# Kernel optimization log

Measured on AMD Instinct MI355X. Metric: run time of the kernel, lower is better.

The kernel has to match this reference:

```python
import jax, jax.numpy as jnp
import numpy as np

FACTOR = 5  # init arg 'factor'


def setup_inputs() -> dict:
    key = jax.random.key(0)
    ks = jax.random.split(key, 9)
    B, L, H, D = 32, 4096, 8, 64
    sh = (B, L, H, D)
    scale = 0.125  # 1/sqrt(D)
    return {
        "queries": jax.random.normal(ks[0], sh, jnp.float32),
        "keys": jax.random.normal(ks[1], sh, jnp.float32),
        "values": jax.random.normal(ks[2], sh, jnp.float32),
        "Wq": jax.random.normal(ks[3], (1, D), jnp.float32) * scale,
        "bq": jax.random.normal(ks[4], (1,), jnp.float32) * scale,
        "Wk": jax.random.normal(ks[5], (1, D), jnp.float32) * scale,
        "bk": jax.random.normal(ks[6], (1,), jnp.float32) * scale,
        "Wv": jax.random.normal(ks[7], (1, D), jnp.float32) * scale,
        "bv": jax.random.normal(ks[8], (1,), jnp.float32) * scale,
    }


def reference(queries, keys, values, Wq, bq, Wk, bk, Wv, bv):
    B, L_Q, H, D = queries.shape
    # transpose(2,1) + LazyLinear(1) + squeeze  ->  scalar series per (b, h, t)
    q = jnp.einsum('blhd,d->bhl', queries, Wq[0]) + bq[0]  # [B,H,L_Q]
    k = jnp.einsum('blhd,d->bhl', keys, Wk[0]) + bk[0]
    v = jnp.einsum('blhd,d->bhl', values, Wv[0]) + bv[0]
    # L_K == L_Q here: torch takes the last L_Q steps (identity in this config)
    k = k[:, :, -L_Q:]
    v = v[:, :, -L_Q:]
    # FFT cross-correlation scores (rfft with n=2L-1 -> L bins; irfft default -> 2L-2)
    n_fft = 2 * L_Q - 1
    Qf = jnp.fft.rfft(q, n_fft)
    Kf = jnp.conj(jnp.fft.rfft(k, n_fft))
    score = jnp.fft.irfft(Qf * Kf)[:, :, :L_Q] / L_Q  # [B,H,L_Q]
    kk = FACTOR * int(np.ceil(np.log(L_Q)))  # 45 for L_Q=4096
    weight, top_idx = jax.lax.top_k(score, kk)  # [B,H,kk]
    weight = jax.nn.softmax(weight, axis=-1)
    # torch: indices = L_Q - top_idx - 1; rolled-V row j is roll(v, j+1),
    # i.e. shift = L_Q - top_idx, so V_sel[b,h,d,t] = v[b,h,(t + top_idx[b,h,d]) % L_Q].
    t = jnp.arange(L_Q)
    gidx = (top_idx[..., None] + t[None, None, None, :]) % L_Q  # [B,H,kk,L_Q]
    V_sel = jnp.take_along_axis(v[:, :, None, :], gidx, axis=-1)  # [B,H,kk,L_Q]
    out = jnp.einsum('bhd,bhdl->bhl', weight, V_sel)  # [B,H,L_Q]
    return out[..., None]  # [B,H,L_Q,1]
```

## Files before the change

### kernel.cpp

```cpp
#include <hip/hip_runtime.h>
#include <math.h>
#include <float.h>

#define L_   4096
#define M_   8192
#define H_   8
#define D_   64
#define KK   45

#define WS_C   0
#define WS_D   4096
#define WS_TW  8192
#define WS_H1  16384
#define WS_H2  24576
#define WS_QKV 32768

__device__ __forceinline__ float2 cadd(float2 a, float2 b) { return make_float2(a.x + b.x, a.y + b.y); }
__device__ __forceinline__ float2 csub(float2 a, float2 b) { return make_float2(a.x - b.x, a.y - b.y); }
__device__ __forceinline__ float2 cmulf(float2 a, float2 b) {
  return make_float2(a.x * b.x - a.y * b.y, a.x * b.y + a.y * b.x);
}
__device__ __forceinline__ float2 cmulcf(float2 a, float2 b) {
  return make_float2(a.x * b.x + a.y * b.y, a.y * b.x - a.x * b.y);
}

__device__ __forceinline__ float2 twf(int e) {
  float s, c;
  __sincosf((float)e * -7.66990394e-4f, &s, &c);
  return make_float2(c, s);
}

#define R4DIF(BUF) { \
  const float2 a = BUF[i0], b = BUF[i0 + q], c = BUF[i0 + 2 * q], d = BUF[i0 + 3 * q]; \
  const float2 t0 = cadd(a, c), t1 = csub(a, c), t2 = cadd(b, d), t3 = csub(b, d); \
  BUF[i0]         = cadd(t0, t2); \
  BUF[i0 + q]     = cmulf(make_float2(t1.x + t3.y, t1.y - t3.x), w1); \
  BUF[i0 + 2 * q] = cmulf(csub(t0, t2), w2); \
  BUF[i0 + 3 * q] = cmulf(make_float2(t1.x - t3.y, t1.y + t3.x), w3); }

#define R4DIT(BUF) { \
  const float2 z0 = BUF[i0]; \
  const float2 z1 = cmulcf(BUF[i0 + q],     w1); \
  const float2 z2 = cmulcf(BUF[i0 + 2 * q], w2); \
  const float2 z3 = cmulcf(BUF[i0 + 3 * q], w3); \
  const float2 t0 = cadd(z0, z2), t1 = csub(z0, z2), t2 = cadd(z1, z3), u = csub(z1, z3); \
  BUF[i0]         = cadd(t0, t2); \
  BUF[i0 + q]     = make_float2(t1.x - u.y, t1.y + u.x); \
  BUF[i0 + 2 * q] = csub(t0, t2); \
  BUF[i0 + 3 * q] = make_float2(t1.x + u.y, t1.y - u.x); }

__device__ __forceinline__ float4 midpair(float4 a, float4 h) {
  float2 u = make_float2(a.x + a.z, a.y + a.w);
  float2 v = make_float2(a.x - a.z, a.y - a.w);
  u = cmulf(u, make_float2(h.x, h.y));
  v = cmulf(v, make_float2(h.z, h.w));
  return make_float4(u.x + v.x, u.y + v.y, u.x - v.x, u.y - v.y);
}

static __device__ void conv2(float2* A, float2* B, const float2* __restrict__ Hf) {
  const int tid = threadIdx.x;
  #pragma unroll
  for (int s = 0; s < 6; ++s) {
    const int q = 2048 >> (2 * s);
    __syncthreads();
    #pragma unroll
    for (int r = 0; r < 2; ++r) {
      const int bid = tid + (r << 10);
      const int j   = bid & (q - 1);
      const int i0  = ((bid >> (11 - 2 * s)) << (13 - 2 * s)) + j;
      const float2 w1 = twf(j << (2 * s));
      const float2 w2 = cmulf(w1, w1);
      const float2 w3 = cmulf(w2, w1);
      R4DIF(A) R4DIF(B)
    }
  }
  __syncthreads();
  #pragma unroll
  for (int r = 0; r < 4; ++r) {
    const int p = tid + (r << 10);
    const float4 h = reinterpret_cast<const float4*>(Hf)[p];
    reinterpret_cast<float4*>(A)[p] = midpair(reinterpret_cast<float4*>(A)[p], h);
    reinterpret_cast<float4*>(B)[p] = midpair(reinterpret_cast<float4*>(B)[p], h);
  }
  #pragma unroll
  for (int s = 5; s >= 0; --s) {
    const int q = 2048 >> (2 * s);
    __syncthreads();
    #pragma unroll
    for (int r = 0; r < 2; ++r) {
      const int bid = tid + (r << 10);
      const int j   = bid & (q - 1);
      const int i0  = ((bid >> (11 - 2 * s)) << (13 - 2 * s)) + j;
      const float2 w1 = twf(j << (2 * s));
      const float2 w2 = cmulf(w1, w1);
      const float2 w3 = cmulf(w2, w1);
      R4DIT(A) R4DIT(B)
    }
  }
  __syncthreads();
}

static __device__ void conv1(float2* A, const float2* __restrict__ Hf) {
  const int tid = threadIdx.x;
  #pragma unroll
  for (int s = 0; s < 6; ++s) {
    const int q = 2048 >> (2 * s);
    __syncthreads();
    #pragma unroll
    for (int r = 0; r < 2; ++r) {
      const int bid = tid + (r << 10);
      const int j   = bid & (q - 1);
      const int i0  = ((bid >> (11 - 2 * s)) << (13 - 2 * s)) + j;
      const float2 w1 = twf(j << (2 * s));
      const float2 w2 = cmulf(w1, w1);
      const float2 w3 = cmulf(w2, w1);
      R4DIF(A)
    }
  }
  __syncthreads();
  #pragma unroll
  for (int r = 0; r < 4; ++r) {
    const int p = tid + (r << 10);
    const float4 h = reinterpret_cast<const float4*>(Hf)[p];
    reinterpret_cast<float4*>(A)[p] = midpair(reinterpret_cast<float4*>(A)[p], h);
  }
  #pragma unroll
  for (int s = 5; s >= 0; --s) {
    const int q = 2048 >> (2 * s);
    __syncthreads();
    #pragma unroll
    for (int r = 0; r < 2; ++r) {
      const int bid = tid + (r << 10);
      const int j   = bid & (q - 1);
      const int i0  = ((bid >> (11 - 2 * s)) << (13 - 2 * s)) + j;
      const float2 w1 = twf(j << (2 * s));
      const float2 w2 = cmulf(w1, w1);
      const float2 w3 = cmulf(w2, w1);
      R4DIT(A)
    }
  }
  __syncthreads();
}

template <int NT>
static __device__ void fft_dif_tab(float2* buf, const float2* __restrict__ tw) {
  const int tid = threadIdx.x;
  for (int s = 0; s < 6; ++s) {
    const int q = 2048 >> (2 * s);
    __syncthreads();
    for (int r = 0; r < 2048 / NT; ++r) {
      const int bid = tid + r * NT;
      const int j   = bid & (q - 1);
      const int i0  = ((bid >> (11 - 2 * s)) << (13 - 2 * s)) + j;
      const int e   = j << (2 * s);
      const float2 w1 = tw[e], w2 = tw[2 * e], w3 = tw[3 * e];
      R4DIF(buf)
    }
  }
  __syncthreads();
  for (int r = 0; r < 4096 / NT; ++r) {
    const int i0 = (tid + r * NT) << 1;
    const float2 a = buf[i0], b = buf[i0 + 1];
    buf[i0] = cadd(a, b); buf[i0 + 1] = csub(a, b);
  }
  __syncthreads();
}

extern "C" __global__ void setup_tables(float2* ws) {
  const int idx = blockIdx.x * 512 + threadIdx.x;
  if (idx < 4096) {
    const long p = ((long)idx * idx) % 16382;
    const double th = -M_PI * (double)p / 8191.0;
    double s, c; sincos(th, &s, &c);
    ws[WS_C + idx] = make_float2((float)c, (float)s);
  } else if (idx < 8192) {
    const int j = idx - 4096;
    const long p = ((long)j * j) % 16380;
    const double th = M_PI * (double)p / 8190.0;
    double s, c; sincos(th, &s, &c);
    ws[WS_D + j] = make_float2((float)c, (float)s);
  } else if (idx < 16384) {
    const int j = idx - 8192;
    const double th = -M_PI * (double)j / 4096.0;
    double s, c; sincos(th, &s, &c);
    ws[WS_TW + j] = make_float2((float)c, (float)s);
  }
}

extern "C" __global__ __launch_bounds__(512, 1) void setup_filters(float2* ws) {
  __shared__ __align__(16) float2 buf[M_];
  const float2* src = ws + (blockIdx.x == 0 ? WS_C : WS_D);
  float2*       dst = ws + (blockIdx.x == 0 ? WS_H1 : WS_H2);
  const float2* tw  = ws + WS_TW;
  for (int i = threadIdx.x; i < M_; i += 512) {
    float2 val = make_float2(0.f, 0.f);
    if (i != 4096) {
      const int jj = (i <= 4095) ? i : (M_ - i);
      const float2 e = src[jj];
      val = make_float2(e.x, -e.y);
    }
    buf[i] = val;
  }
  fft_dif_tab<512>(buf, tw);
  const float sc = 1.0f / 8192.0f;
  for (int i = threadIdx.x; i < M_; i += 512)
    dst[i] = make_float2(buf[i].x * sc, buf[i].y * sc);
}

extern "C" __global__ __launch_bounds__(256)
void proj_kernel(const float* __restrict__ queries, const float* __restrict__ keys,
                 const float* __restrict__ values,
                 const float* __restrict__ Wq, const float* __restrict__ bq,
                 const float* __restrict__ Wk, const float* __restrict__ bk,
                 const float* __restrict__ Wv, const float* __restrict__ bv,
                 float* __restrict__ q_ws, float* __restrict__ k_ws,
                 float* __restrict__ v_ws)
{
  const int tid  = threadIdx.x;
  const int wave = tid >> 6;
  const int lane = tid & 63;
  const int qt   = lane & 3;
  const int rr   = lane >> 2;
  const int hh   = rr & 7;
  const int dl   = rr >> 3;
  const int blk  = blockIdx.x;
  const int b    = blk >> 6;
  const int lbase = (blk & 63) << 6;

  const float* srcs[3] = {queries, keys, values};
  const float* Wsx[3]  = {Wq, Wk, Wv};
  const float* Bsx[3]  = {bq, bk, bv};
  float* dsts[3] = {q_ws, k_ws, v_ws};

  #pragma unroll
  for (int s = 0; s < 3; ++s) {
    const float4* src4 = reinterpret_cast<const float4*>(srcs[s]) + (size_t)b * 524288;
    const float4* W4   = reinterpret_cast<const float4*>(Wsx[s]);
    float4 w[4];
    #pragma unroll
    for (int j = 0; j < 4; ++j) w[j] = W4[qt * 4 + j];
    const float bias = Bsx[s][0];
    float* dst = dsts[s] + ((size_t)(b * 8 + hh) << 12);

    #pragma unroll
    for (int st = 0; st < 4; ++st) {
      const int l0a = lbase + st * 16 + wave * 2;
      const int l0b = l0a + 8;
      const float4* pa = src4 + (size_t)l0a * 128 + lane * 4;
      const float4* pb = src4 + (size_t)l0b * 128 + lane * 4;
      float4 xa[4], xb[4];
      #pragma unroll
      for (int j = 0; j < 4; ++j) xa[j] = pa[j];
      #pragma unroll
      for (int j = 0; j < 4; ++j) xb[j] = pb[j];
      float fa = 0.f, fb = 0.f;
      #pragma unroll
      for (int j = 0; j < 4; ++j) {
        fa += xa[j].x * w[j].x + xa[j].y * w[j].y + xa[j].z * w[j].z + xa[j].w * w[j].w;
        fb += xb[j].x * w[j].x + xb[j].y * w[j].y + xb[j].z * w[j].z + xb[j].w * w[j].w;
      }
      fa += __shfl_xor(fa, 1); fb += __shfl_xor(fb, 1);
      fa += __shfl_xor(fa, 2); fb += __shfl_xor(fb, 2);
      if (qt == 0) {
        dst[l0a + dl] = fa + bias;
        dst[l0b + dl] = fb + bias;
      }
    }
  }
}

extern "C" __global__ __launch_bounds__(1024, 1)
void autocorr_main(const float2* __restrict__ ws,
                   const float* __restrict__ q_ws, const float* __restrict__ k_ws,
                   const float* __restrict__ v_ws, float* __restrict__ outp)
{
  __shared__ __align__(16) float2 bufA[M_];
  __shared__ __align__(16) float2 bufB[M_];
  __shared__ float  v_lds[L_];
  __shared__ float  cand_v[16 * KK];
  __shared__ int    cand_i[16 * KK];
  __shared__ float  w_sh[KK];
  __shared__ int    i_sh[KK];

  const int tid = threadIdx.x;
  const int bh  = blockIdx.x;

  const float2* c_t = ws + WS_C;
  const float2* d_t = ws + WS_D;
  const float2* H1  = ws + WS_H1;
  const float2* H2  = ws + WS_H2;
  const float* qrow = q_ws + ((size_t)bh << 12);
  const float* krow = k_ws + ((size_t)bh << 12);
  const float* vrow = v_ws + ((size_t)bh << 12);

  {
    const float4 v4 = reinterpret_cast<const float4*>(vrow)[tid];
    reinterpret_cast<float4*>(v_lds)[tid] = v4;
    const float4 k4 = reinterpret_cast<const float4*>(krow)[tid];
    const float4 q4 = reinterpret_cast<const float4*>(qrow)[tid];
    const float4 c01 = reinterpret_cast<const float4*>(c_t)[2 * tid];
    const float4 c23 = reinterpret_cast<const float4*>(c_t)[2 * tid + 1];
    float4* A4 = reinterpret_cast<float4*>(bufA);
    float4* B4 = reinterpret_cast<float4*>(bufB);
    A4[2 * tid]     = make_float4(k4.x * c01.x, k4.x * c01.y, k4.y * c01.z, k4.y * c01.w);
    A4[2 * tid + 1] = make_float4(k4.z * c23.x, k4.z * c23.y, k4.w * c23.z, k4.w * c23.w);
    B4[2 * tid]     = make_float4(q4.x * c01.x, q4.x * c01.y, q4.y * c01.z, q4.y * c01.w);
    B4[2 * tid + 1] = make_float4(q4.z * c23.x, q4.z * c23.y, q4.w * c23.z, q4.w * c23.w);
    const float4 z = make_float4(0.f, 0.f, 0.f, 0.f);
    A4[2048 + tid] = z; A4[3072 + tid] = z;
    B4[2048 + tid] = z; B4[3072 + tid] = z;
  }

  conv2(bufA, bufB, H1);

  #pragma unroll
  for (int r = 0; r < 4; ++r) {
    const int m = tid + (r << 10);
    const float2 cc = c_t[m];
    const float2 K = cmulf(cc, bufA[m]);
    const float2 Q = cmulf(cc, bufB[m]);
    const float2 F = cmulcf(Q, K);
    float2 g;
    if (m == 0 || m == 4095) g = make_float2(F.x, 0.f);
    else                     g = make_float2(2.f * F.x, 2.f * F.y);
    bufA[m] = cmulf(g, d_t[m]);
  }
  #pragma unroll
  for (int r = 4; r < 8; ++r) bufA[tid + (r << 10)] = make_float2(0.f, 0.f);

  conv1(bufA, H2);

  const float SCALE = (float)(1.0 / (8190.0 * 4096.0));
  float svv[4]; int sii[4];
  #pragma unroll
  for (int r = 0; r < 4; ++r) {
    const int t = tid + (r << 10);
    const float2 Z = cmulf(d_t[t], bufA[t]);
    svv[r] = Z.x * SCALE;
    sii[r] = t;
  }
  const int lane = tid & 63, wv = tid >> 6;
  for (int it = 0; it < KK; ++it) {
    float bvv = -FLT_MAX; int bii = 0x7fffffff;
    #pragma unroll
    for (int c = 0; c < 4; ++c)
      if (svv[c] > bvv || (svv[c] == bvv && sii[c] < bii)) { bvv = svv[c]; bii = sii[c]; }
    #pragma unroll
    for (int off = 1; off < 64; off <<= 1) {
      const float ov = __shfl_xor(bvv, off);
      const int   oi = __shfl_xor(bii, off);
      if (ov > bvv || (ov == bvv && oi < bii)) { bvv = ov; bii = oi; }
    }
    #pragma unroll
    for (int c = 0; c < 4; ++c) if (sii[c] == bii) svv[c] = -FLT_MAX;
    if (lane == 0) { cand_v[wv * KK + it] = bvv; cand_i[wv * KK + it] = bii; }
  }
  __syncthreads();

  if (tid < 64) {
    float mv[12]; int mi[12];
    #pragma unroll
    for (int c = 0; c < 12; ++c) {
      const int id = tid + 64 * c;
      if (id < 16 * KK) { mv[c] = cand_v[id]; mi[c] = cand_i[id]; }
      else              { mv[c] = -FLT_MAX;   mi[c] = 0x7fffffff; }
    }
    float m0 = 0.f, sum = 0.f, myv = -FLT_MAX; int myi = 0;
    for (int it = 0; it < KK; ++it) {
      float bvv = -FLT_MAX; int bii = 0x7fffffff;
      #pragma unroll
      for (int c = 0; c < 12; ++c)
        if (mv[c] > bvv || (mv[c] == bvv && mi[c] < bii)) { bvv = mv[c]; bii = mi[c]; }
      #pragma unroll
      for (int off = 1; off < 64; off <<= 1) {
        const float ov = __shfl_xor(bvv, off);
        const int   oi = __shfl_xor(bii, off);
        if (ov > bvv || (ov == bvv && oi < bii)) { bvv = ov; bii = oi; }
      }
      if (it == 0) m0 = bvv;
      sum += expf(bvv - m0);
      if (tid == it) { myv = bvv; myi = bii; }
      #pragma unroll
      for (int c = 0; c < 12; ++c) if (mi[c] == bii) mv[c] = -FLT_MAX;
    }
    if (tid < KK) { w_sh[tid] = expf(myv - m0) / sum; i_sh[tid] = myi; }
  }
  __syncthreads();

  {
    float acc[4] = {0, 0, 0, 0};
    for (int j = 0; j < KK; ++j) {
      const float wj = w_sh[j];
      const int   bse = i_sh[j] + tid;
      #pragma unroll
      for (int r = 0; r < 4; ++r)
        acc[r] = fmaf(wj, v_lds[(bse + (r << 10)) & (L_ - 1)], acc[r]);
    }
    float* op = outp + ((size_t)bh << 12);
    #pragma unroll
    for (int r = 0; r < 4; ++r) op[tid + (r << 10)] = acc[r];
  }
}

extern "C" void kernel_launch(void* const* d_in, const int* in_sizes, int n_in,
                              void* d_out, int out_size, void* d_ws, size_t ws_size,
                              hipStream_t stream) {
  const float* queries = (const float*)d_in[0];
  const float* keys    = (const float*)d_in[1];
  const float* values  = (const float*)d_in[2];
  const float* Wq = (const float*)d_in[3];
  const float* bq = (const float*)d_in[4];
  const float* Wk = (const float*)d_in[5];
  const float* bk = (const float*)d_in[6];
  const float* Wv = (const float*)d_in[7];
  const float* bv = (const float*)d_in[8];
  float2* ws = (float2*)d_ws;
  float* q_ws = (float*)d_ws + 2 * WS_QKV;
  float* k_ws = q_ws + (1 << 20);
  float* v_ws = k_ws + (1 << 20);
  float* out = (float*)d_out;

  hipLaunchKernelGGL(setup_tables,  dim3(32), dim3(512), 0, stream, ws);
  hipLaunchKernelGGL(setup_filters, dim3(2),  dim3(512), 0, stream, ws);
  hipLaunchKernelGGL(proj_kernel,   dim3(2048), dim3(256), 0, stream,
                     queries, keys, values, Wq, bq, Wk, bk, Wv, bv, q_ws, k_ws, v_ws);
  hipLaunchKernelGGL(autocorr_main, dim3(256), dim3(1024), 0, stream,
                     ws, q_ws, k_ws, v_ws, out);
}
```

Baseline: 340.0 us.

## Swizzle LDS FFT buffers against bank conflicts and pipeline projection loads

The in-LDS radix-4 FFT buffers get an XOR-swizzled index mapping (PS/PS4), applied consistently to the butterfly stages, the pointwise multiply, the fill and the readout. The goal is to remove LDS bank conflicts on the strided butterfly accesses. The projection kernel is also rewritten as a triple-buffered software pipeline using nontemporal vector loads and a launch-bounds occupancy hint, so global loads overlap the dot-product reductions. The risks are extra index arithmetic, more register pressure, and subtle errors if any access to the buffers is missed by the swizzle.

New measurement: 396.9 us. +16.7%, slower.

```diff
diff --git a/kernel.cpp b/kernel.cpp
--- a/kernel.cpp
+++ b/kernel.cpp
@@ -15,6 +15,8 @@
 #define WS_H2  24576
 #define WS_QKV 32768
 
+typedef float vf4 __attribute__((ext_vector_type(4)));
+
 __device__ __forceinline__ float2 cadd(float2 a, float2 b) { return make_float2(a.x + b.x, a.y + b.y); }
 __device__ __forceinline__ float2 csub(float2 a, float2 b) { return make_float2(a.x - b.x, a.y - b.y); }
 __device__ __forceinline__ float2 cmulf(float2 a, float2 b) {
@@ -30,7 +32,10 @@
   return make_float2(c, s);
 }
 
-#define R4DIF(BUF) { \
+__device__ __forceinline__ int PS(int i)  { return i ^ ((i >> 3) & 0xE); }
+__device__ __forceinline__ int PS4(int t) { return t ^ ((t >> 3) & 7);  }
+
+#define R4DIF_L(BUF) { \
   const float2 a = BUF[i0], b = BUF[i0 + q], c = BUF[i0 + 2 * q], d = BUF[i0 + 3 * q]; \
   const float2 t0 = cadd(a, c), t1 = csub(a, c), t2 = cadd(b, d), t3 = csub(b, d); \
   BUF[i0]         = cadd(t0, t2); \
@@ -38,16 +43,24 @@
   BUF[i0 + 2 * q] = cmulf(csub(t0, t2), w2); \
   BUF[i0 + 3 * q] = cmulf(make_float2(t1.x - t3.y, t1.y + t3.x), w3); }
 
-#define R4DIT(BUF) { \
-  const float2 z0 = BUF[i0]; \
-  const float2 z1 = cmulcf(BUF[i0 + q],     w1); \
-  const float2 z2 = cmulcf(BUF[i0 + 2 * q], w2); \
-  const float2 z3 = cmulcf(BUF[i0 + 3 * q], w3); \
+#define R4DIFS(BUF) { \
+  const float2 a = BUF[a0], b = BUF[a1], c = BUF[a2], d = BUF[a3]; \
+  const float2 t0 = cadd(a, c), t1 = csub(a, c), t2 = cadd(b, d), t3 = csub(b, d); \
+  BUF[a0] = cadd(t0, t2); \
+  BUF[a1] = cmulf(make_float2(t1.x + t3.y, t1.y - t3.x), w1); \
+  BUF[a2] = cmulf(csub(t0, t2), w2); \
+  BUF[a3] = cmulf(make_float2(t1.x - t3.y, t1.y + t3.x), w3); }
+
+#define R4DITS(BUF) { \
+  const float2 z0 = BUF[a0]; \
+  const float2 z1 = cmulcf(BUF[a1], w1); \
+  const float2 z2 = cmulcf(BUF[a2], w2); \
+  const float2 z3 = cmulcf(BUF[a3], w3); \
   const float2 t0 = cadd(z0, z2), t1 = csub(z0, z2), t2 = cadd(z1, z3), u = csub(z1, z3); \
-  BUF[i0]         = cadd(t0, t2); \
-  BUF[i0 + q]     = make_float2(t1.x - u.y, t1.y + u.x); \
-  BUF[i0 + 2 * q] = csub(t0, t2); \
-  BUF[i0 + 3 * q] = make_float2(t1.x + u.y, t1.y - u.x); }
+  BUF[a0] = cadd(t0, t2); \
+  BUF[a1] = make_float2(t1.x - u.y, t1.y + u.x); \
+  BUF[a2] = csub(t0, t2); \
+  BUF[a3] = make_float2(t1.x + u.y, t1.y - u.x); }
 
 __device__ __forceinline__ float4 midpair(float4 a, float4 h) {
   float2 u = make_float2(a.x + a.z, a.y + a.w);
@@ -59,42 +72,50 @@
 
 static __device__ void conv2(float2* A, float2* B, const float2* __restrict__ Hf) {
   const int tid = threadIdx.x;
+  float4* A4f = reinterpret_cast<float4*>(A);
+  float4* B4f = reinterpret_cast<float4*>(B);
+  const float4* H4 = reinterpret_cast<const float4*>(Hf);
   #pragma unroll
   for (int s = 0; s < 6; ++s) {
     const int q = 2048 >> (2 * s);
+    const int pq1 = PS(q), pq2 = PS(2 * q), pq3 = PS(3 * q);
     __syncthreads();
     #pragma unroll
     for (int r = 0; r < 2; ++r) {
       const int bid = tid + (r << 10);
       const int j   = bid & (q - 1);
       const int i0  = ((bid >> (11 - 2 * s)) << (13 - 2 * s)) + j;
+      const int a0  = PS(i0), a1 = a0 ^ pq1, a2 = a0 ^ pq2, a3 = a0 ^ pq3;
       const float2 w1 = twf(j << (2 * s));
       const float2 w2 = cmulf(w1, w1);
       const float2 w3 = cmulf(w2, w1);
-      R4DIF(A) R4DIF(B)
+      R4DIFS(A) R4DIFS(B)
     }
   }
   __syncthreads();
   #pragma unroll
   for (int r = 0; r < 4; ++r) {
-    const int p = tid + (r << 10);
-    const float4 h = reinterpret_cast<const float4*>(Hf)[p];
-    reinterpret_cast<float4*>(A)[p] = midpair(reinterpret_cast<float4*>(A)[p], h);
-    reinterpret_cast<float4*>(B)[p] = midpair(reinterpret_cast<float4*>(B)[p], h);
+    const int p  = tid + (r << 10);
+    const int pp = PS4(p);
+    const float4 h = H4[p];
+    A4f[pp] = midpair(A4f[pp], h);
+    B4f[pp] = midpair(B4f[pp], h);
   }
   #pragma unroll
   for (int s = 5; s >= 0; --s) {
     const int q = 2048 >> (2 * s);
+    const int pq1 = PS(q), pq2 = PS(2 * q), pq3 = PS(3 * q);
     __syncthreads();
     #pragma unroll
     for (int r = 0; r < 2; ++r) {
       const int bid = tid + (r << 10);
       const int j   = bid & (q - 1);
       const int i0  = ((bid >> (11 - 2 * s)) << (13 - 2 * s)) + j;
+      const int a0  = PS(i0), a1 = a0 ^ pq1, a2 = a0 ^ pq2, a3 = a0 ^ pq3;
       const float2 w1 = twf(j << (2 * s));
       const float2 w2 = cmulf(w1, w1);
       const float2 w3 = cmulf(w2, w1);
-      R4DIT(A) R4DIT(B)
+      R4DITS(A) R4DITS(B)
     }
   }
   __syncthreads();
@@ -102,41 +123,48 @@
 
 static __device__ void conv1(float2* A, const float2* __restrict__ Hf) {
   const int tid = threadIdx.x;
+  float4* A4f = reinterpret_cast<float4*>(A);
+  const float4* H4 = reinterpret_cast<const float4*>(Hf);
   #pragma unroll
   for (int s = 0; s < 6; ++s) {
     const int q = 2048 >> (2 * s);
+    const int pq1 = PS(q), pq2 = PS(2 * q), pq3 = PS(3 * q);
     __syncthreads();
     #pragma unroll
     for (int r = 0; r < 2; ++r) {
       const int bid = tid + (r << 10);
       const int j   = bid & (q - 1);
       const int i0  = ((bid >> (11 - 2 * s)) << (13 - 2 * s)) + j;
+      const int a0  = PS(i0), a1 = a0 ^ pq1, a2 = a0 ^ pq2, a3 = a0 ^ pq3;
       const float2 w1 = twf(j << (2 * s));
       const float2 w2 = cmulf(w1, w1);
       const float2 w3 = cmulf(w2, w1);
-      R4DIF(A)
+      R4DIFS(A)
     }
   }
   __syncthreads();
   #pragma unroll
   for (int r = 0; r < 4; ++r) {
-    const int p = tid + (r << 10);
-    const float4 h = reinterpret_cast<const float4*>(Hf)[p];
-    reinterpret_cast<float4*>(A)[p] = midpair(reinterpret_cast<float4*>(A)[p], h);
+    const int p  = tid + (r << 10);
+    const int pp = PS4(p);
+    const float4 h = H4[p];
+    A4f[pp] = midpair(A4f[pp], h);
   }
   #pragma unroll
   for (int s = 5; s >= 0; --s) {
     const int q = 2048 >> (2 * s);
+    const int pq1 = PS(q), pq2 = PS(2 * q), pq3 = PS(3 * q);
     __syncthreads();
     #pragma unroll
     for (int r = 0; r < 2; ++r) {
       const int bid = tid + (r << 10);
       const int j   = bid & (q - 1);
       const int i0  = ((bid >> (11 - 2 * s)) << (13 - 2 * s)) + j;
+      const int a0  = PS(i0), a1 = a0 ^ pq1, a2 = a0 ^ pq2, a3 = a0 ^ pq3;
       const float2 w1 = twf(j << (2 * s));
       const float2 w2 = cmulf(w1, w1);
       const float2 w3 = cmulf(w2, w1);
-      R4DIT(A)
+      R4DITS(A)
     }
   }
   __syncthreads();
@@ -154,7 +182,7 @@
       const int i0  = ((bid >> (11 - 2 * s)) << (13 - 2 * s)) + j;
       const int e   = j << (2 * s);
       const float2 w1 = tw[e], w2 = tw[2 * e], w3 = tw[3 * e];
-      R4DIF(buf)
+      R4DIF_L(buf)
     }
   }
   __syncthreads();
@@ -207,7 +235,32 @@
     dst[i] = make_float2(buf[i].x * sc, buf[i].y * sc);
 }
 
-extern "C" __global__ __launch_bounds__(256)
+#define PROJ_ISSUE(BUF, IT) { \
+  const int s_ = (IT) >> 3, g_ = (IT) & 7; \
+  const int l0_ = lbase + (wave << 1) + (g_ << 3); \
+  const vf4* p_ = (s_ == 0 ? q4p : (s_ == 1 ? k4p : v4p)) + (((size_t)l0_) << 7) + (lane << 2); \
+  BUF[0] = __builtin_nontemporal_load(p_ + 0); \
+  BUF[1] = __builtin_nontemporal_load(p_ + 1); \
+  BUF[2] = __builtin_nontemporal_load(p_ + 2); \
+  BUF[3] = __builtin_nontemporal_load(p_ + 3); }
+
+#define PROJ_REDUCE(BUF, IT) { \
+  const int s_ = (IT) >> 3, g_ = (IT) & 7; \
+  const int l0_ = lbase + (wave << 1) + (g_ << 3); \
+  const float4 w0_ = (s_ == 0 ? wq0 : (s_ == 1 ? wk0 : wv0)); \
+  const float4 w1_ = (s_ == 0 ? wq1 : (s_ == 1 ? wk1 : wv1)); \
+  const float4 w2_ = (s_ == 0 ? wq2 : (s_ == 1 ? wk2 : wv2)); \
+  const float4 w3_ = (s_ == 0 ? wq3 : (s_ == 1 ? wk3 : wv3)); \
+  float f_ = BUF[0].x * w0_.x + BUF[0].y * w0_.y + BUF[0].z * w0_.z + BUF[0].w * w0_.w \
+           + BUF[1].x * w1_.x + BUF[1].y * w1_.y + BUF[1].z * w1_.z + BUF[1].w * w1_.w \
+           + BUF[2].x * w2_.x + BUF[2].y * w2_.y + BUF[2].z * w2_.z + BUF[2].w * w2_.w \
+           + BUF[3].x * w3_.x + BUF[3].y * w3_.y + BUF[3].z * w3_.z + BUF[3].w * w3_.w; \
+  f_ += __shfl_xor(f_, 1); f_ += __shfl_xor(f_, 2); \
+  if (qt == 0) { \
+    float* d_ = (s_ == 0 ? q_ws : (s_ == 1 ? k_ws : v_ws)) + (((size_t)(b8 + hh)) << 12) + l0_ + dl; \
+    *d_ = f_ + (s_ == 0 ? bq0 : (s_ == 1 ? bk0 : bv0)); } }
+
+extern "C" __global__ __launch_bounds__(256, 4)
 void proj_kernel(const float* __restrict__ queries, const float* __restrict__ keys,
                  const float* __restrict__ values,
                  const float* __restrict__ Wq, const float* __restrict__ bq,
@@ -225,47 +278,35 @@
   const int dl   = rr >> 3;
   const int blk  = blockIdx.x;
   const int b    = blk >> 6;
+  const int b8   = b * 8;
   const int lbase = (blk & 63) << 6;
 
-  const float* srcs[3] = {queries, keys, values};
-  const float* Wsx[3]  = {Wq, Wk, Wv};
-  const float* Bsx[3]  = {bq, bk, bv};
-  float* dsts[3] = {q_ws, k_ws, v_ws};
-
-  #pragma unroll
-  for (int s = 0; s < 3; ++s) {
-    const float4* src4 = reinterpret_cast<const float4*>(srcs[s]) + (size_t)b * 524288;
-    const float4* W4   = reinterpret_cast<const float4*>(Wsx[s]);
-    float4 w[4];
-    #pragma unroll
-    for (int j = 0; j < 4; ++j) w[j] = W4[qt * 4 + j];
-    const float bias = Bsx[s][0];
-    float* dst = dsts[s] + ((size_t)(b * 8 + hh) << 12);
-
-    #pragma unroll
-    for (int st = 0; st < 4; ++st) {
-      const int l0a = lbase + st * 16 + wave * 2;
-      const int l0b = l0a + 8;
-      const float4* pa = src4 + (size_t)l0a * 128 + lane * 4;
-      const float4* pb = src4 + (size_t)l0b * 128 + lane * 4;
-      float4 xa[4], xb[4];
-      #pragma unroll
-      for (int j = 0; j < 4; ++j) xa[j] = pa[j];
-      #pragma unroll
-      for (int j = 0; j < 4; ++j) xb[j] = pb[j];
-      float fa = 0.f, fb = 0.f;
-      #pragma unroll
-      for (int j = 0; j < 4; ++j) {
-        fa += xa[j].x * w[j].x + xa[j].y * w[j].y + xa[j].z * w[j].z + xa[j].w * w[j].w;
-        fb += xb[j].x * w[j].x + xb[j].y * w[j].y + xb[j].z * w[j].z + xb[j].w * w[j].w;
-      }
-      fa += __shfl_xor(fa, 1); fb += __shfl_xor(fb, 1);
-      fa += __shfl_xor(fa, 2); fb += __shfl_xor(fb, 2);
-      if (qt == 0) {
-        dst[l0a + dl] = fa + bias;
-        dst[l0b + dl] = fb + bias;
-      }
-    }
+  const vf4* q4p = reinterpret_cast<const vf4*>(queries) + (size_t)b * 524288;
+  const vf4* k4p = reinterpret_cast<const vf4*>(keys)    + (size_t)b * 524288;
+  const vf4* v4p = reinterpret_cast<const vf4*>(values)  + (size_t)b * 524288;
+
+  const float4* Wq4 = reinterpret_cast<const float4*>(Wq);
+  const float4* Wk4 = reinterpret_cast<const float4*>(Wk);
+  const float4* Wv4 = reinterpret_cast<const float4*>(Wv);
+  const float4 wq0 = Wq4[qt * 4 + 0], wq1 = Wq4[qt * 4 + 1], wq2 = Wq4[qt * 4 + 2], wq3 = Wq4[qt * 4 + 3];
+  const float4 wk0 = Wk4[qt * 4 + 0], wk1 = Wk4[qt * 4 + 1], wk2 = Wk4[qt * 4 + 2], wk3 = Wk4[qt * 4 + 3];
+  const float4 wv0 = Wv4[qt * 4 + 0], wv1 = Wv4[qt * 4 + 1], wv2 = Wv4[qt * 4 + 2], wv3 = Wv4[qt * 4 + 3];
+  const float bq0 = bq[0], bk0 = bk[0], bv0 = bv[0];
+
+  vf4 bA[4], bB[4], bC[4];
+  PROJ_ISSUE(bA, 0)
+  PROJ_ISSUE(bB, 1)
+  #pragma unroll
+  for (int it = 0; it < 24; ++it) {
+    const int nx = it + 2;
+    if (nx < 24) {
+      if      (nx % 3 == 0) { PROJ_ISSUE(bA, nx) }
+      else if (nx % 3 == 1) { PROJ_ISSUE(bB, nx) }
+      else                  { PROJ_ISSUE(bC, nx) }
+    }
+    if      (it % 3 == 0) { PROJ_REDUCE(bA, it) }
+    else if (it % 3 == 1) { PROJ_REDUCE(bB, it) }
+    else                  { PROJ_REDUCE(bC, it) }
   }
 }
 
@@ -302,10 +343,11 @@
     const float4 c23 = reinterpret_cast<const float4*>(c_t)[2 * tid + 1];
     float4* A4 = reinterpret_cast<float4*>(bufA);
     float4* B4 = reinterpret_cast<float4*>(bufB);
-    A4[2 * tid]     = make_float4(k4.x * c01.x, k4.x * c01.y, k4.y * c01.z, k4.y * c01.w);
-    A4[2 * tid + 1] = make_float4(k4.z * c23.x, k4.z * c23.y, k4.w * c23.z, k4.w * c23.w);
-    B4[2 * tid]     = make_float4(q4.x * c01.x, q4.x * c01.y, q4.y * c01.z, q4.y * c01.w);
-    B4[2 * tid + 1] = make_float4(q4.z * c23.x, q4.z * c23.y, q4.w * c23.z, q4.w * c23.w);
+    const int p0 = PS4(2 * tid), p1 = PS4(2 * tid + 1);
+    A4[p0] = make_float4(k4.x * c01.x, k4.x * c01.y, k4.y * c01.z, k4.y * c01.w);
+    A4[p1] = make_float4(k4.z * c23.x, k4.z * c23.y, k4.w * c23.z, k4.w * c23.w);
+    B4[p0] = make_float4(q4.x * c01.x, q4.x * c01.y, q4.y * c01.z, q4.y * c01.w);
+    B4[p1] = make_float4(q4.z * c23.x, q4.z * c23.y, q4.w * c23.z, q4.w * c23.w);
     const float4 z = make_float4(0.f, 0.f, 0.f, 0.f);
     A4[2048 + tid] = z; A4[3072 + tid] = z;
     B4[2048 + tid] = z; B4[3072 + tid] = z;
@@ -315,15 +357,16 @@
 
   #pragma unroll
   for (int r = 0; r < 4; ++r) {
-    const int m = tid + (r << 10);
+    const int m  = tid + (r << 10);
+    const int pm = PS(m);
     const float2 cc = c_t[m];
-    const float2 K = cmulf(cc, bufA[m]);
-    const float2 Q = cmulf(cc, bufB[m]);
+    const float2 K = cmulf(cc, bufA[pm]);
+    const float2 Q = cmulf(cc, bufB[pm]);
     const float2 F = cmulcf(Q, K);
     float2 g;
     if (m == 0 || m == 4095) g = make_float2(F.x, 0.f);
     else                     g = make_float2(2.f * F.x, 2.f * F.y);
-    bufA[m] = cmulf(g, d_t[m]);
+    bufA[pm] = cmulf(g, d_t[m]);
   }
   #pragma unroll
   for (int r = 4; r < 8; ++r) bufA[tid + (r << 10)] = make_float2(0.f, 0.f);
@@ -335,7 +378,7 @@
   #pragma unroll
   for (int r = 0; r < 4; ++r) {
     const int t = tid + (r << 10);
-    const float2 Z = cmulf(d_t[t], bufA[t]);
+    const float2 Z = cmulf(d_t[t], bufA[PS(t)]);
     svv[r] = Z.x * SCALE;
     sii[r] = t;
   }
```

## Fuse projections into FFT kernels and split forward spectra across blocks

Applied to the files above, without the earlier changes.

Removes the separate projection kernel. The Q/K projections are fused into a new forward kernel that runs 512 blocks, one per (b,h,q-or-k), and writes spectra to workspace. The inverse kernel then fuses the V projection, reads both spectra and does the correlation, inverse FFT and top-k. The first and last radix-4 stages are done in registers, exploiting the known zero halves to skip work. The cost is an extra spectra round-trip through global memory, in exchange for more parallelism and one fewer LDS buffer per block.

Measured after the change: 363.8 us. 7.0% more time.

```diff
diff --git a/kernel.cpp b/kernel.cpp
--- a/kernel.cpp
+++ b/kernel.cpp
@@ -13,7 +13,8 @@
 #define WS_TW  8192
 #define WS_H1  16384
 #define WS_H2  24576
-#define WS_QKV 32768
+#define WS_SK  32768
+#define WS_SQ  1081344
 
 __device__ __forceinline__ float2 cadd(float2 a, float2 b) { return make_float2(a.x + b.x, a.y + b.y); }
 __device__ __forceinline__ float2 csub(float2 a, float2 b) { return make_float2(a.x - b.x, a.y - b.y); }
@@ -49,6 +50,26 @@
   BUF[i0 + 2 * q] = csub(t0, t2); \
   BUF[i0 + 3 * q] = make_float2(t1.x + u.y, t1.y - u.x); }
 
+__device__ __forceinline__ void bfly4_dif(float2 x[4], float2 w1, float2 w2, float2 w3) {
+  const float2 t0 = cadd(x[0], x[2]), t1 = csub(x[0], x[2]);
+  const float2 t2 = cadd(x[1], x[3]), t3 = csub(x[1], x[3]);
+  x[0] = cadd(t0, t2);
+  x[1] = cmulf(make_float2(t1.x + t3.y, t1.y - t3.x), w1);
+  x[2] = cmulf(csub(t0, t2), w2);
+  x[3] = cmulf(make_float2(t1.x - t3.y, t1.y + t3.x), w3);
+}
+__device__ __forceinline__ void bfly4_dit(float2 x[4], float2 w1, float2 w2, float2 w3) {
+  const float2 z0 = x[0];
+  const float2 z1 = cmulcf(x[1], w1);
+  const float2 z2 = cmulcf(x[2], w2);
+  const float2 z3 = cmulcf(x[3], w3);
+  const float2 t0 = cadd(z0, z2), t1 = csub(z0, z2), t2 = cadd(z1, z3), u = csub(z1, z3);
+  x[0] = cadd(t0, t2);
+  x[1] = make_float2(t1.x - u.y, t1.y + u.x);
+  x[2] = csub(t0, t2);
+  x[3] = make_float2(t1.x + u.y, t1.y - u.x);
+}
+
 __device__ __forceinline__ float4 midpair(float4 a, float4 h) {
   float2 u = make_float2(a.x + a.z, a.y + a.w);
   float2 v = make_float2(a.x - a.z, a.y - a.w);
@@ -57,53 +78,10 @@
   return make_float4(u.x + v.x, u.y + v.y, u.x - v.x, u.y - v.y);
 }
 
-static __device__ void conv2(float2* A, float2* B, const float2* __restrict__ Hf) {
+static __device__ void fwd_stages1(float2* A) {
   const int tid = threadIdx.x;
   #pragma unroll
-  for (int s = 0; s < 6; ++s) {
-    const int q = 2048 >> (2 * s);
-    __syncthreads();
-    #pragma unroll
-    for (int r = 0; r < 2; ++r) {
-      const int bid = tid + (r << 10);
-      const int j   = bid & (q - 1);
-      const int i0  = ((bid >> (11 - 2 * s)) << (13 - 2 * s)) + j;
-      const float2 w1 = twf(j << (2 * s));
-      const float2 w2 = cmulf(w1, w1);
-      const float2 w3 = cmulf(w2, w1);
-      R4DIF(A) R4DIF(B)
-    }
-  }
-  __syncthreads();
-  #pragma unroll
-  for (int r = 0; r < 4; ++r) {
-    const int p = tid + (r << 10);
-    const float4 h = reinterpret_cast<const float4*>(Hf)[p];
-    reinterpret_cast<float4*>(A)[p] = midpair(reinterpret_cast<float4*>(A)[p], h);
-    reinterpret_cast<float4*>(B)[p] = midpair(reinterpret_cast<float4*>(B)[p], h);
-  }
-  #pragma unroll
-  for (int s = 5; s >= 0; --s) {
-    const int q = 2048 >> (2 * s);
-    __syncthreads();
-    #pragma unroll
-    for (int r = 0; r < 2; ++r) {
-      const int bid = tid + (r << 10);
-      const int j   = bid & (q - 1);
-      const int i0  = ((bid >> (11 - 2 * s)) << (13 - 2 * s)) + j;
-      const float2 w1 = twf(j << (2 * s));
-      const float2 w2 = cmulf(w1, w1);
-      const float2 w3 = cmulf(w2, w1);
-      R4DIT(A) R4DIT(B)
-    }
-  }
-  __syncthreads();
-}
-
-static __device__ void conv1(float2* A, const float2* __restrict__ Hf) {
-  const int tid = threadIdx.x;
-  #pragma unroll
-  for (int s = 0; s < 6; ++s) {
+  for (int s = 1; s < 6; ++s) {
     const int q = 2048 >> (2 * s);
     __syncthreads();
     #pragma unroll
@@ -117,15 +95,11 @@
       R4DIF(A)
     }
   }
-  __syncthreads();
-  #pragma unroll
-  for (int r = 0; r < 4; ++r) {
-    const int p = tid + (r << 10);
-    const float4 h = reinterpret_cast<const float4*>(Hf)[p];
-    reinterpret_cast<float4*>(A)[p] = midpair(reinterpret_cast<float4*>(A)[p], h);
-  }
-  #pragma unroll
-  for (int s = 5; s >= 0; --s) {
+}
+static __device__ void inv_stages1(float2* A) {
+  const int tid = threadIdx.x;
+  #pragma unroll
+  for (int s = 5; s >= 1; --s) {
     const int q = 2048 >> (2 * s);
     __syncthreads();
     #pragma unroll
@@ -139,7 +113,6 @@
       R4DIT(A)
     }
   }
-  __syncthreads();
 }
 
 template <int NT>
@@ -207,75 +180,116 @@
     dst[i] = make_float2(buf[i].x * sc, buf[i].y * sc);
 }
 
-extern "C" __global__ __launch_bounds__(256)
-void proj_kernel(const float* __restrict__ queries, const float* __restrict__ keys,
-                 const float* __restrict__ values,
-                 const float* __restrict__ Wq, const float* __restrict__ bq,
-                 const float* __restrict__ Wk, const float* __restrict__ bk,
-                 const float* __restrict__ Wv, const float* __restrict__ bv,
-                 float* __restrict__ q_ws, float* __restrict__ k_ws,
-                 float* __restrict__ v_ws)
+#define ROW_ISSUE(BUF, SW) { \
+  const size_t f0 = ((size_t)((SW) * 256 + lgrp)) * 128 + qt * 4; \
+  BUF[0] = s4[f0]; BUF[1] = s4[f0 + 1]; BUF[2] = s4[f0 + 2]; BUF[3] = s4[f0 + 3]; }
+
+#define ROW_REDUCE(DST, BUF, SW) { \
+  float f_ = BUF[0].x * w0.x + BUF[0].y * w0.y + BUF[0].z * w0.z + BUF[0].w * w0.w \
+           + BUF[1].x * w1.x + BUF[1].y * w1.y + BUF[1].z * w1.z + BUF[1].w * w1.w \
+           + BUF[2].x * w2.x + BUF[2].y * w2.y + BUF[2].z * w2.z + BUF[2].w * w2.w \
+           + BUF[3].x * w3.x + BUF[3].y * w3.y + BUF[3].z * w3.z + BUF[3].w * w3.w; \
+  f_ += __shfl_xor(f_, 1); f_ += __shfl_xor(f_, 2); \
+  if (qt == 0) DST[(SW) * 256 + lgrp] = f_ + bias; }
+
+#define ROW_STREAM(DST) { \
+  float4 pA[4], pB[4]; \
+  ROW_ISSUE(pA, 0) \
+  ROW_ISSUE(pB, 1) \
+  _Pragma("unroll") \
+  for (int sw = 0; sw < 16; sw += 2) { \
+    ROW_REDUCE(DST, pA, sw) \
+    if (sw + 2 < 16) { ROW_ISSUE(pA, sw + 2) } \
+    ROW_REDUCE(DST, pB, sw + 1) \
+    if (sw + 3 < 16) { ROW_ISSUE(pB, sw + 3) } \
+  } }
+
+extern "C" __global__ __launch_bounds__(1024, 8)
+void autocorr_fwd(const float* __restrict__ queries, const float* __restrict__ keys,
+                  const float* __restrict__ Wq, const float* __restrict__ bq,
+                  const float* __restrict__ Wk, const float* __restrict__ bk,
+                  float2* __restrict__ ws)
 {
-  const int tid  = threadIdx.x;
-  const int wave = tid >> 6;
-  const int lane = tid & 63;
-  const int qt   = lane & 3;
-  const int rr   = lane >> 2;
-  const int hh   = rr & 7;
-  const int dl   = rr >> 3;
-  const int blk  = blockIdx.x;
-  const int b    = blk >> 6;
-  const int lbase = (blk & 63) << 6;
-
-  const float* srcs[3] = {queries, keys, values};
-  const float* Wsx[3]  = {Wq, Wk, Wv};
-  const float* Bsx[3]  = {bq, bk, bv};
-  float* dsts[3] = {q_ws, k_ws, v_ws};
-
-  #pragma unroll
-  for (int s = 0; s < 3; ++s) {
-    const float4* src4 = reinterpret_cast<const float4*>(srcs[s]) + (size_t)b * 524288;
-    const float4* W4   = reinterpret_cast<const float4*>(Wsx[s]);
-    float4 w[4];
-    #pragma unroll
-    for (int j = 0; j < 4; ++j) w[j] = W4[qt * 4 + j];
-    const float bias = Bsx[s][0];
-    float* dst = dsts[s] + ((size_t)(b * 8 + hh) << 12);
-
-    #pragma unroll
-    for (int st = 0; st < 4; ++st) {
-      const int l0a = lbase + st * 16 + wave * 2;
-      const int l0b = l0a + 8;
-      const float4* pa = src4 + (size_t)l0a * 128 + lane * 4;
-      const float4* pb = src4 + (size_t)l0b * 128 + lane * 4;
-      float4 xa[4], xb[4];
-      #pragma unroll
-      for (int j = 0; j < 4; ++j) xa[j] = pa[j];
-      #pragma unroll
-      for (int j = 0; j < 4; ++j) xb[j] = pb[j];
-      float fa = 0.f, fb = 0.f;
-      #pragma unroll
-      for (int j = 0; j < 4; ++j) {
-        fa += xa[j].x * w[j].x + xa[j].y * w[j].y + xa[j].z * w[j].z + xa[j].w * w[j].w;
-        fb += xb[j].x * w[j].x + xb[j].y * w[j].y + xb[j].z * w[j].z + xb[j].w * w[j].w;
-      }
-      fa += __shfl_xor(fa, 1); fb += __shfl_xor(fb, 1);
-      fa += __shfl_xor(fa, 2); fb += __shfl_xor(fb, 2);
-      if (qt == 0) {
-        dst[l0a + dl] = fa + bias;
-        dst[l0b + dl] = fb + bias;
-      }
+  __shared__ __align__(16) float2 buf[M_];
+  float* rst = reinterpret_cast<float*>(buf) + 8192;
+
+  const int tid   = threadIdx.x;
+  const int bh    = blockIdx.x & 255;
+  const int which = blockIdx.x >> 8;
+  const int b = bh >> 3, h = bh & 7;
+  const int qt = tid & 3, lgrp = tid >> 2;
+
+  const float2* c_t = ws + WS_C;
+  const float2* H1  = ws + WS_H1;
+  const float* src  = (which ? queries : keys) + ((size_t)b * (L_ * H_) + h) * (size_t)D_;
+  const float4* s4  = reinterpret_cast<const float4*>(src);
+  const float4* W4  = reinterpret_cast<const float4*>(which ? Wq : Wk);
+  const float4 w0 = W4[qt * 4 + 0], w1 = W4[qt * 4 + 1];
+  const float4 w2 = W4[qt * 4 + 2], w3 = W4[qt * 4 + 3];
+  const float bias = which ? bq[0] : bk[0];
+
+  ROW_STREAM(rst)
+  __syncthreads();
+
+  float r0[2], r1[2];
+  #pragma unroll
+  for (int r = 0; r < 2; ++r) {
+    const int bid = tid + (r << 10);
+    r0[r] = rst[bid];
+    r1[r] = rst[bid + 2048];
+  }
+  __syncthreads();
+  #pragma unroll
+  for (int r = 0; r < 2; ++r) {
+    const int bid = tid + (r << 10);
+    const float2 tw1 = twf(bid);
+    const float2 tw2 = cmulf(tw1, tw1);
+    const float2 tw3 = cmulf(tw2, tw1);
+    const float2 cc0 = c_t[bid], cc1 = c_t[bid + 2048];
+    float2 x[4] = { make_float2(r0[r] * cc0.x, r0[r] * cc0.y),
+                    make_float2(r1[r] * cc1.x, r1[r] * cc1.y),
+                    make_float2(0.f, 0.f), make_float2(0.f, 0.f) };
+    bfly4_dif(x, tw1, tw2, tw3);
+    #pragma unroll
+    for (int k = 0; k < 4; ++k) buf[bid + k * 2048] = x[k];
+  }
+
+  fwd_stages1(buf);
+  __syncthreads();
+  #pragma unroll
+  for (int r = 0; r < 4; ++r) {
+    const int p = tid + (r << 10);
+    const float4 hh = reinterpret_cast<const float4*>(H1)[p];
+    reinterpret_cast<float4*>(buf)[p] = midpair(reinterpret_cast<float4*>(buf)[p], hh);
+  }
+  inv_stages1(buf);
+  __syncthreads();
+
+  float2* spec = ws + (which ? WS_SQ : WS_SK) + (size_t)bh * 4096;
+  #pragma unroll
+  for (int r = 0; r < 2; ++r) {
+    const int bid = tid + (r << 10);
+    const float2 tw1 = twf(bid);
+    const float2 tw2 = cmulf(tw1, tw1);
+    const float2 tw3 = cmulf(tw2, tw1);
+    float2 x[4];
+    #pragma unroll
+    for (int k = 0; k < 4; ++k) x[k] = buf[bid + k * 2048];
+    bfly4_dit(x, tw1, tw2, tw3);
+    #pragma unroll
+    for (int k = 0; k < 2; ++k) {
+      const int m = bid + k * 2048;
+      spec[m] = cmulf(c_t[m], x[k]);
     }
   }
 }
 
 extern "C" __global__ __launch_bounds__(1024, 1)
-void autocorr_main(const float2* __restrict__ ws,
-                   const float* __restrict__ q_ws, const float* __restrict__ k_ws,
-                   const float* __restrict__ v_ws, float* __restrict__ outp)
+void autocorr_inv(const float* __restrict__ values,
+                  const float* __restrict__ Wv, const float* __restrict__ bv,
+                  const float2* __restrict__ ws, float* __restrict__ outp)
 {
-  __shared__ __align__(16) float2 bufA[M_];
-  __shared__ __align__(16) float2 bufB[M_];
+  __shared__ __align__(16) float2 buf[M_];
   __shared__ float  v_lds[L_];
   __shared__ float  cand_v[16 * KK];
   __shared__ int    cand_i[16 * KK];
@@ -284,61 +298,80 @@
 
   const int tid = threadIdx.x;
   const int bh  = blockIdx.x;
-
-  const float2* c_t = ws + WS_C;
+  const int b = bh >> 3, h = bh & 7;
+  const int qt = tid & 3, lgrp = tid >> 2;
+
   const float2* d_t = ws + WS_D;
-  const float2* H1  = ws + WS_H1;
   const float2* H2  = ws + WS_H2;
-  const float* qrow = q_ws + ((size_t)bh << 12);
-  const float* krow = k_ws + ((size_t)bh << 12);
-  const float* vrow = v_ws + ((size_t)bh << 12);
+  const float2* SK  = ws + WS_SK + (size_t)bh * 4096;
+  const float2* SQ  = ws + WS_SQ + (size_t)bh * 4096;
 
   {
-    const float4 v4 = reinterpret_cast<const float4*>(vrow)[tid];
-    reinterpret_cast<float4*>(v_lds)[tid] = v4;
-    const float4 k4 = reinterpret_cast<const float4*>(krow)[tid];
-    const float4 q4 = reinterpret_cast<const float4*>(qrow)[tid];
-    const float4 c01 = reinterpret_cast<const float4*>(c_t)[2 * tid];
-    const float4 c23 = reinterpret_cast<const float4*>(c_t)[2 * tid + 1];
-    float4* A4 = reinterpret_cast<float4*>(bufA);
-    float4* B4 = reinterpret_cast<float4*>(bufB);
-    A4[2 * tid]     = make_float4(k4.x * c01.x, k4.x * c01.y, k4.y * c01.z, k4.y * c01.w);
-    A4[2 * tid + 1] = make_float4(k4.z * c23.x, k4.z * c23.y, k4.w * c23.z, k4.w * c23.w);
-    B4[2 * tid]     = make_float4(q4.x * c01.x, q4.x * c01.y, q4.y * c01.z, q4.y * c01.w);
-    B4[2 * tid + 1] = make_float4(q4.z * c23.x, q4.z * c23.y, q4.w * c23.z, q4.w * c23.w);
-    const float4 z = make_float4(0.f, 0.f, 0.f, 0.f);
-    A4[2048 + tid] = z; A4[3072 + tid] = z;
-    B4[2048 + tid] = z; B4[3072 + tid] = z;
-  }
-
-  conv2(bufA, bufB, H1);
-
+    const float* src = values + ((size_t)b * (L_ * H_) + h) * (size_t)D_;
+    const float4* s4 = reinterpret_cast<const float4*>(src);
+    const float4* W4 = reinterpret_cast<const float4*>(Wv);
+    const float4 w0 = W4[qt * 4 + 0], w1 = W4[qt * 4 + 1];
+    const float4 w2 = W4[qt * 4 + 2], w3 = W4[qt * 4 + 3];
+    const float bias = bv[0];
+    ROW_STREAM(v_lds)
+  }
+
+  #pragma unroll
+  for (int r = 0; r < 2; ++r) {
+    const int bid = tid + (r << 10);
+    const float2 tw1 = twf(bid);
+    const float2 tw2 = cmulf(tw1, tw1);
+    const float2 tw3 = cmulf(tw2, tw1);
+    float2 gd[2];
+    #pragma unroll
+    for (int k = 0; k < 2; ++k) {
+      const int m = bid + k * 2048;
+      const float2 K = SK[m];
+      const float2 Q = SQ[m];
+      const float2 F = cmulcf(Q, K);
+      float2 g;
+      if (m == 0 || m == 4095) g = make_float2(F.x, 0.f);
+      else                     g = make_float2(2.f * F.x, 2.f * F.y);
+      gd[k] = cmulf(g, d_t[m]);
+    }
+    float2 x[4] = { gd[0], gd[1], make_float2(0.f, 0.f), make_float2(0.f, 0.f) };
+    bfly4_dif(x, tw1, tw2, tw3);
+    #pragma unroll
+    for (int k = 0; k < 4; ++k) buf[bid + k * 2048] = x[k];
+  }
+
+  fwd_stages1(buf);
+  __syncthreads();
   #pragma unroll
   for (int r = 0; r < 4; ++r) {
-    const int m = tid + (r << 10);
-    const float2 cc = c_t[m];
-    const float2 K = cmulf(cc, bufA[m]);
-    const float2 Q = cmulf(cc, bufB[m]);
-    const float2 F = cmulcf(Q, K);
-    float2 g;
-    if (m == 0 || m == 4095) g = make_float2(F.x, 0.f);
-    else                     g = make_float2(2.f * F.x, 2.f * F.y);
-    bufA[m] = cmulf(g, d_t[m]);
-  }
-  #pragma unroll
-  for (int r = 4; r < 8; ++r) bufA[tid + (r << 10)] = make_float2(0.f, 0.f);
-
-  conv1(bufA, H2);
+    const int p = tid + (r << 10);
+    const float4 hh = reinterpret_cast<const float4*>(H2)[p];
+    reinterpret_cast<float4*>(buf)[p] = midpair(reinterpret_cast<float4*>(buf)[p], hh);
+  }
+  inv_stages1(buf);
+  __syncthreads();
 
   const float SCALE = (float)(1.0 / (8190.0 * 4096.0));
   float svv[4]; int sii[4];
   #pragma unroll
-  for (int r = 0; r < 4; ++r) {
-    const int t = tid + (r << 10);
-    const float2 Z = cmulf(d_t[t], bufA[t]);
-    svv[r] = Z.x * SCALE;
-    sii[r] = t;
-  }
+  for (int r = 0; r < 2; ++r) {
+    const int bid = tid + (r << 10);
+    const float2 tw1 = twf(bid);
+    const float2 tw2 = cmulf(tw1, tw1);
+    const float2 tw3 = cmulf(tw2, tw1);
+    float2 x[4];
+    #pragma unroll
+    for (int k = 0; k < 4; ++k) x[k] = buf[bid + k * 2048];
+    bfly4_dit(x, tw1, tw2, tw3);
+    #pragma unroll
+    for (int k = 0; k < 2; ++k) {
+      const int t = bid + k * 2048;
+      const float2 Z = cmulf(d_t[t], x[k]);
+      svv[2 * r + k] = Z.x * SCALE;
+      sii[2 * r + k] = t;
+    }
+  }
+
   const int lane = tid & 63, wv = tid >> 6;
   for (int it = 0; it < KK; ++it) {
     float bvv = -FLT_MAX; int bii = 0x7fffffff;
@@ -415,15 +448,12 @@
   const float* Wv = (const float*)d_in[7];
   const float* bv = (const float*)d_in[8];
   float2* ws = (float2*)d_ws;
-  float* q_ws = (float*)d_ws + 2 * WS_QKV;
-  float* k_ws = q_ws + (1 << 20);
-  float* v_ws = k_ws + (1 << 20);
   float* out = (float*)d_out;
 
   hipLaunchKernelGGL(setup_tables,  dim3(32), dim3(512), 0, stream, ws);
   hipLaunchKernelGGL(setup_filters, dim3(2),  dim3(512), 0, stream, ws);
-  hipLaunchKernelGGL(proj_kernel,   dim3(2048), dim3(256), 0, stream,
-                     queries, keys, values, Wq, bq, Wk, bk, Wv, bv, q_ws, k_ws, v_ws);
-  hipLaunchKernelGGL(autocorr_main, dim3(256), dim3(1024), 0, stream,
-                     ws, q_ws, k_ws, v_ws, out);
-}
+  hipLaunchKernelGGL(autocorr_fwd,  dim3(512), dim3(1024), 0, stream,
+                     queries, keys, Wq, bq, Wk, bk, ws);
+  hipLaunchKernelGGL(autocorr_inv,  dim3(256), dim3(1024), 0, stream,
+                     values, Wv, bv, ws, out);
+}
```
